# Kernel optimization log

Hardware: AMD Instinct MI355X
Metric: run time of the kernel (lower is better)

Reference implementation:

```python
import jax, jax.numpy as jnp
import numpy as np

N = 100000
E = 3200000
D_IN = 128
HEADS = 4
OUT_CH = 64


def setup_inputs() -> dict:
    key = jax.random.key(0)
    kx, ke, kw, kb = jax.random.split(key, 4)
    x = jax.random.normal(kx, (N, D_IN), dtype=jnp.float32)
    edge_index = jax.random.randint(ke, (2, E), 0, N, dtype=jnp.int64)
    # nn.Linear(in_channels, out_channels*heads): weight [out, in] in torch; store as [in, out] for x @ W
    W = jax.random.normal(kw, (D_IN, OUT_CH * HEADS), dtype=jnp.float32) * (1.0 / np.sqrt(D_IN))
    b = jax.random.normal(kb, (OUT_CH * HEADS,), dtype=jnp.float32) * 0.01
    return {"x": x, "edge_index": edge_index, "W": W, "b": b}


def reference(x, edge_index, W, b):
    src, dst = edge_index[0], edge_index[1]
    n = x.shape[0]
    # scatter-add of gathered src features into dst rows (segment sum)
    agg = jax.ops.segment_sum(x[src], dst, num_segments=n)  # [N, D_IN]
    count = jax.ops.segment_sum(jnp.ones((src.shape[0], 1), x.dtype), dst, num_segments=n)  # [N, 1]
    agg = agg / (count + 1e-8)
    # linear on (x + agg); view to [N, heads*out_channels] is a no-op reshape
    return (x + agg) @ W + b
```

## Files before the change

### kernel.cpp

```cpp
#include <hip/hip_runtime.h>

#define N_NODES 100000
#define D_IN 128
#define D_OUT 256
#define NBLK 256
#define NBKT 256
#define BSH  9
#define BNODES 512
#define NBUCKETS ((N_NODES + BNODES - 1) / BNODES)
#define CAP  19456

typedef __attribute__((ext_vector_type(8))) short short8_t;
typedef __attribute__((ext_vector_type(4))) float f32x4;

__device__ inline unsigned short f2bf_rne(float f) {
    unsigned u = __float_as_uint(f);
    u += 0x7fffu + ((u >> 16) & 1u);
    return (unsigned short)(u >> 16);
}

__global__ __launch_bounds__(256) void convert_kernel(
    const float* __restrict__ x, ushort* __restrict__ xb, int n4)
{
    int i = blockIdx.x * 256 + threadIdx.x;
    if (i < n4) {
        float4 v = ((const float4*)x)[i];
        ushort4 r;
        r.x = f2bf_rne(v.x); r.y = f2bf_rne(v.y);
        r.z = f2bf_rne(v.z); r.w = f2bf_rne(v.w);
        ((ushort4*)xb)[i] = r;
    }
}

__global__ __launch_bounds__(256) void wfrag_kernel(
    const float* __restrict__ W, short8_t* __restrict__ wfrag)
{
    int tid  = blockIdx.x * 256 + threadIdx.x;
    int lane = tid & 63;
    int fi   = tid >> 6;
    int ks   = fi >> 4, nt = fi & 15;
    int k0   = ks * 32 + (lane >> 4) * 8;
    int col  = nt * 16 + (lane & 15);
    short8_t v;
    #pragma unroll
    for (int e = 0; e < 8; e++)
        v[e] = (short)f2bf_rne(W[(size_t)(k0 + e) * D_OUT + col]);
    wfrag[tid] = v;
}

__global__ __launch_bounds__(256) void binA_hist(
    const int* __restrict__ dst, int* __restrict__ blockHist, int E, int chunk)
{
    __shared__ int h[NBKT];
    int b = blockIdx.x, t = threadIdx.x;
    h[t] = 0;
    __syncthreads();
    int e0 = b * chunk, e1 = min(e0 + chunk, E);
    for (int e = e0 + t; e < e1; e += 256)
        atomicAdd(&h[dst[e] >> BSH], 1);
    __syncthreads();
    blockHist[b * NBKT + t] = h[t];
}

__global__ __launch_bounds__(256) void binA_scan(
    int* __restrict__ blockHist, int* __restrict__ bucketTotal)
{
    __shared__ int wsum[4];
    int bucket = blockIdx.x;
    int t = threadIdx.x, lane = t & 63, w = t >> 6;
    int v = blockHist[t * NBKT + bucket];
    int s = v;
    #pragma unroll
    for (int d = 1; d < 64; d <<= 1) {
        int u = __shfl_up(s, d);
        if (lane >= d) s += u;
    }
    if (lane == 63) wsum[w] = s;
    __syncthreads();
    int wo = 0;
    for (int j = 0; j < w; j++) wo += wsum[j];
    blockHist[t * NBKT + bucket] = wo + s - v;
    if (t == 255) {
        int tot = 0;
        for (int j = 0; j < 4; j++) tot += wsum[j];
        bucketTotal[bucket] = tot;
    }
}

__global__ __launch_bounds__(256) void binA_scanbase(
    const int* __restrict__ bucketTotal, int* __restrict__ bucketBase)
{
    __shared__ int wsum[4];
    int t = threadIdx.x, lane = t & 63, w = t >> 6;
    int v = bucketTotal[t];
    int s = v;
    #pragma unroll
    for (int d = 1; d < 64; d <<= 1) {
        int u = __shfl_up(s, d);
        if (lane >= d) s += u;
    }
    if (lane == 63) wsum[w] = s;
    __syncthreads();
    int wo = 0;
    for (int j = 0; j < w; j++) wo += wsum[j];
    bucketBase[t] = wo + s - v;
}

__global__ __launch_bounds__(256) void binA_scatter(
    const int* __restrict__ src, const int* __restrict__ dst,
    const int* __restrict__ blockHist, const int* __restrict__ bucketBase,
    unsigned* __restrict__ pairs, int E, int chunk)
{
    __shared__ int offs[NBKT];
    int b = blockIdx.x, t = threadIdx.x;
    offs[t] = bucketBase[t] + blockHist[b * NBKT + t];
    __syncthreads();
    int e0 = b * chunk, e1 = min(e0 + chunk, E);
    for (int e = e0 + t; e < e1; e += 256) {
        int d = dst[e];
        int bin = d >> BSH;
        int pos = atomicAdd(&offs[bin], 1);
        pairs[pos] = ((unsigned)(d & (BNODES - 1)) << 17) | (unsigned)src[e];
    }
}

__global__ __launch_bounds__(256) void binB_sort(
    unsigned* __restrict__ pairs, const int* __restrict__ bucketBase,
    int* __restrict__ offs_g, int* __restrict__ deg_g)
{
    __shared__ unsigned stage[CAP];
    __shared__ int hist[BNODES];
    __shared__ int rank[BNODES];
    __shared__ int wsum[4];

    int b = blockIdx.x, t = threadIdx.x, lane = t & 63, w = t >> 6;
    int e0 = bucketBase[b], e1 = bucketBase[b + 1];
    int cnt = e1 - e0;
    if (cnt > CAP) cnt = CAP;

    hist[t] = 0; hist[t + 256] = 0;
    __syncthreads();

    for (int i = t; i < cnt; i += 256) {
        unsigned p = pairs[e0 + i];
        stage[i] = p;
        atomicAdd(&hist[p >> 17], 1);
    }
    __syncthreads();

    int a0 = hist[t * 2], a1 = hist[t * 2 + 1];
    int v = a0 + a1;
    int s = v;
    #pragma unroll
    for (int d = 1; d < 64; d <<= 1) {
        int u = __shfl_up(s, d);
        if (lane >= d) s += u;
    }
    if (lane == 63) wsum[w] = s;
    __syncthreads();
    int wo = 0;
    for (int j = 0; j < w; j++) wo += wsum[j];
    int excl = wo + s - v;

    rank[t * 2]     = excl;
    rank[t * 2 + 1] = excl + a0;
    int node = (b << BSH) + t * 2;
    if (node < N_NODES) {
        offs_g[node] = e0 + excl;
        deg_g[node]  = a0;
    }
    if (node + 1 < N_NODES) {
        offs_g[node + 1] = e0 + excl + a0;
        deg_g[node + 1]  = a1;
    }
    __syncthreads();

    for (int i = t; i < cnt; i += 256) {
        unsigned p = stage[i];
        int pos = atomicAdd(&rank[p >> 17], 1);
        pairs[e0 + pos] = p & 0x1FFFFu;
    }
}

template <bool USE_BF16>
__global__ __launch_bounds__(256) void fused_kernel(
    const float* __restrict__ x,
    const ushort* __restrict__ xb,
    const int* __restrict__ offs,
    const int* __restrict__ deg,
    const int* __restrict__ sorted_src,
    const short8_t* __restrict__ wfrag,
    const float* __restrict__ b,
    float* __restrict__ out)
{
    __shared__ __align__(16) ushort shb[16 * D_IN];

    int n0   = blockIdx.x * 16;
    int t    = threadIdx.x;
    int lane = t & 63;
    int w    = t >> 6;

    for (int nn = 0; nn < 4; nn++) {
        int nl = w * 4 + nn;
        int n  = n0 + nl;
        int start = offs[n];
        int d     = deg[n];
        float accx = 0.0f, accy = 0.0f;
        for (int base = 0; base < d; base += 64) {
            int m = d - base; if (m > 64) m = 64;
            int id = (lane < m) ? sorted_src[start + base + lane] : 0;
            int j = 0;
            for (; j + 4 <= m; j += 4) {
                int s0 = __builtin_amdgcn_readlane(id, j);
                int s1 = __builtin_amdgcn_readlane(id, j + 1);
                int s2 = __builtin_amdgcn_readlane(id, j + 2);
                int s3 = __builtin_amdgcn_readlane(id, j + 3);
                if (USE_BF16) {
                    ushort2 u0 = ((const ushort2*)(xb + (size_t)s0 * D_IN))[lane];
                    ushort2 u1 = ((const ushort2*)(xb + (size_t)s1 * D_IN))[lane];
                    ushort2 u2 = ((const ushort2*)(xb + (size_t)s2 * D_IN))[lane];
                    ushort2 u3 = ((const ushort2*)(xb + (size_t)s3 * D_IN))[lane];
                    accx += __uint_as_float((unsigned)u0.x << 16)
                          + __uint_as_float((unsigned)u1.x << 16)
                          + __uint_as_float((unsigned)u2.x << 16)
                          + __uint_as_float((unsigned)u3.x << 16);
                    accy += __uint_as_float((unsigned)u0.y << 16)
                          + __uint_as_float((unsigned)u1.y << 16)
                          + __uint_as_float((unsigned)u2.y << 16)
                          + __uint_as_float((unsigned)u3.y << 16);
                } else {
                    float2 v0 = ((const float2*)(x + (size_t)s0 * D_IN))[lane];
                    float2 v1 = ((const float2*)(x + (size_t)s1 * D_IN))[lane];
                    float2 v2 = ((const float2*)(x + (size_t)s2 * D_IN))[lane];
                    float2 v3 = ((const float2*)(x + (size_t)s3 * D_IN))[lane];
                    accx += v0.x + v1.x + v2.x + v3.x;
                    accy += v0.y + v1.y + v2.y + v3.y;
                }
            }
            for (; j < m; j++) {
                int s0 = __builtin_amdgcn_readlane(id, j);
                if (USE_BF16) {
                    ushort2 u0 = ((const ushort2*)(xb + (size_t)s0 * D_IN))[lane];
                    accx += __uint_as_float((unsigned)u0.x << 16);
                    accy += __uint_as_float((unsigned)u0.y << 16);
                } else {
                    float2 v0 = ((const float2*)(x + (size_t)s0 * D_IN))[lane];
                    accx += v0.x; accy += v0.y;
                }
            }
        }
        float invc = 1.0f / ((float)d + 1e-8f);
        float2 xv = ((const float2*)(x + (size_t)n * D_IN))[lane];
        float hx = xv.x + accx * invc;
        float hy = xv.y + accy * invc;
        unsigned hp = ((unsigned)f2bf_rne(hy) << 16) | (unsigned)f2bf_rne(hx);
        unsigned byteoff = ((unsigned)(nl * 256 + lane * 4)) ^ (((unsigned)nl & 7u) << 4);
        *(unsigned*)((char*)shb + byteoff) = hp;
    }
    __syncthreads();

    const int r  = lane & 15;
    const int hi = lane >> 4;

    short8_t afrag[4];
    #pragma unroll
    for (int ks = 0; ks < 4; ks++) {
        unsigned aoff = ((unsigned)(r * 256 + ks * 64 + hi * 16)) ^ (((unsigned)r & 7u) << 4);
        afrag[ks] = *(const short8_t*)((const char*)shb + aoff);
    }

    f32x4 zero = {0.0f, 0.0f, 0.0f, 0.0f};
    f32x4 acc0 = zero, acc1 = zero, acc2 = zero, acc3 = zero;
    const int nt0 = w * 4;
    #pragma unroll
    for (int ks = 0; ks < 4; ks++) {
        short8_t b0 = wfrag[(ks * 16 + nt0    ) * 64 + lane];
        short8_t b1 = wfrag[(ks * 16 + nt0 + 1) * 64 + lane];
        short8_t b2 = wfrag[(ks * 16 + nt0 + 2) * 64 + lane];
        short8_t b3 = wfrag[(ks * 16 + nt0 + 3) * 64 + lane];
        acc0 = __builtin_amdgcn_mfma_f32_16x16x32_bf16(afrag[ks], b0, acc0, 0, 0, 0);
        acc1 = __builtin_amdgcn_mfma_f32_16x16x32_bf16(afrag[ks], b1, acc1, 0, 0, 0);
        acc2 = __builtin_amdgcn_mfma_f32_16x16x32_bf16(afrag[ks], b2, acc2, 0, 0, 0);
        acc3 = __builtin_amdgcn_mfma_f32_16x16x32_bf16(afrag[ks], b3, acc3, 0, 0, 0);
    }

    #pragma unroll
    for (int nt = 0; nt < 4; nt++) {
        f32x4 a = (nt == 0) ? acc0 : (nt == 1) ? acc1 : (nt == 2) ? acc2 : acc3;
        int col = (nt0 + nt) * 16 + r;
        float bias = b[col];
        #pragma unroll
        for (int reg = 0; reg < 4; reg++) {
            int node = n0 + hi * 4 + reg;
            out[(size_t)node * D_OUT + col] = a[reg] + bias;
        }
    }
}

extern "C" void kernel_launch(void* const* d_in, const int* in_sizes, int n_in,
                              void* d_out, int out_size, void* d_ws, size_t ws_size,
                              hipStream_t stream)
{
    const float* x  = (const float*)d_in[0];
    const int*   ei = (const int*)d_in[1];
    const float* W  = (const float*)d_in[2];
    const float* b  = (const float*)d_in[3];
    float*       out = (float*)d_out;

    const int E = in_sizes[1] / 2;
    const int* src = ei;
    const int* dst = ei + E;
    const int chunk = (E + NBLK - 1) / NBLK;

    const size_t xb_bytes   = (size_t)N_NODES * D_IN * 2;
    const size_t pairs_b    = (size_t)E * 4;
    const size_t bh_b       = (size_t)NBLK * NBKT * 4;
    const size_t small_b    = (size_t)NBKT * 4;
    const size_t nodes_b    = (size_t)N_NODES * 4;
    const size_t wf_b       = (size_t)4096 * 16;
    const size_t need_bf16  = xb_bytes + pairs_b + bh_b + 2 * small_b
                            + 2 * nodes_b + wf_b;
    const bool use_bf16 = (ws_size >= need_bf16);

    char* p = (char*)d_ws;
    ushort* xb = nullptr;
    if (use_bf16) { xb = (ushort*)p; p += xb_bytes; }
    unsigned* pairs  = (unsigned*)p;  p += pairs_b;
    int* blockHist   = (int*)p;       p += bh_b;
    int* bucketTotal = (int*)p;       p += small_b;
    int* bucketBase  = (int*)p;       p += small_b;
    int* offs        = (int*)p;       p += nodes_b;
    int* deg         = (int*)p;       p += nodes_b;
    short8_t* wfrag  = (short8_t*)p;

    if (use_bf16) {
        int n4 = N_NODES * D_IN / 4;
        convert_kernel<<<dim3((n4 + 255) / 256), dim3(256), 0, stream>>>(x, xb, n4);
    }
    wfrag_kernel<<<dim3(16), dim3(256), 0, stream>>>(W, wfrag);

    binA_hist    <<<dim3(NBLK), dim3(256), 0, stream>>>(dst, blockHist, E, chunk);
    binA_scan    <<<dim3(NBKT), dim3(256), 0, stream>>>(blockHist, bucketTotal);
    binA_scanbase<<<dim3(1),    dim3(256), 0, stream>>>(bucketTotal, bucketBase);
    binA_scatter <<<dim3(NBLK), dim3(256), 0, stream>>>(
        src, dst, blockHist, bucketBase, pairs, E, chunk);
    binB_sort    <<<dim3(NBUCKETS), dim3(256), 0, stream>>>(
        pairs, bucketBase, offs, deg);

    if (use_bf16)
        fused_kernel<true><<<dim3(N_NODES / 16), dim3(256), 0, stream>>>(
            x, xb, offs, deg, (const int*)pairs, wfrag, b, out);
    else
        fused_kernel<false><<<dim3(N_NODES / 16), dim3(256), 0, stream>>>(
            x, xb, offs, deg, (const int*)pairs, wfrag, b, out);
}
```

Baseline: 405.8 us.

## Stage binning scatter through LDS to coalesce global pair writes

```diff
diff --git a/kernel.cpp b/kernel.cpp
--- a/kernel.cpp
+++ b/kernel.cpp
@@ -9,6 +9,7 @@
 #define BNODES 512
 #define NBUCKETS ((N_NODES + BNODES - 1) / BNODES)
 #define CAP  19456
+#define CAPC 12544
 
 typedef __attribute__((ext_vector_type(8))) short short8_t;
 typedef __attribute__((ext_vector_type(4))) float f32x4;
@@ -111,16 +112,64 @@
     const int* __restrict__ blockHist, const int* __restrict__ bucketBase,
     unsigned* __restrict__ pairs, int E, int chunk)
 {
-    __shared__ int offs[NBKT];
-    int b = blockIdx.x, t = threadIdx.x;
-    offs[t] = bucketBase[t] + blockHist[b * NBKT + t];
-    __syncthreads();
+    __shared__ unsigned stage[CAPC];
+    __shared__ int cnt[NBKT];
+    __shared__ int lofs[NBKT];
+    __shared__ int rankl[NBKT];
+    __shared__ int gcur[NBKT];
+    __shared__ int wsum[4];
+
+    int b = blockIdx.x, t = threadIdx.x, lane = t & 63, w = t >> 6;
     int e0 = b * chunk, e1 = min(e0 + chunk, E);
-    for (int e = e0 + t; e < e1; e += 256) {
-        int d = dst[e];
-        int bin = d >> BSH;
-        int pos = atomicAdd(&offs[bin], 1);
-        pairs[pos] = ((unsigned)(d & (BNODES - 1)) << 17) | (unsigned)src[e];
+
+    gcur[t] = bucketBase[t] + blockHist[b * NBKT + t];
+    __syncthreads();
+
+    for (int c0 = e0; c0 < e1; c0 += CAPC) {
+        int c1 = c0 + CAPC; if (c1 > e1) c1 = e1;
+
+        cnt[t] = 0;
+        __syncthreads();
+
+        for (int e = c0 + t; e < c1; e += 256)
+            atomicAdd(&cnt[dst[e] >> BSH], 1);
+        __syncthreads();
+
+        {
+            int v = cnt[t];
+            int s = v;
+            #pragma unroll
+            for (int d = 1; d < 64; d <<= 1) {
+                int u = __shfl_up(s, d);
+                if (lane >= d) s += u;
+            }
+            if (lane == 63) wsum[w] = s;
+            __syncthreads();
+            int wo = 0;
+            for (int j = 0; j < w; j++) wo += wsum[j];
+            int excl = wo + s - v;
+            lofs[t]  = excl;
+            rankl[t] = excl;
+        }
+        __syncthreads();
+
+        for (int e = c0 + t; e < c1; e += 256) {
+            int d = dst[e];
+            int bin = d >> BSH;
+            int pos = atomicAdd(&rankl[bin], 1);
+            stage[pos] = ((unsigned)(d & (BNODES - 1)) << 17) | (unsigned)src[e];
+        }
+        __syncthreads();
+
+        for (int bin = w; bin < NBKT; bin += 4) {
+            int lo = lofs[bin], c = cnt[bin], g = gcur[bin];
+            for (int i = lane; i < c; i += 64)
+                pairs[g + i] = stage[lo + i];
+        }
+        __syncthreads();
+
+        gcur[t] += cnt[t];
+        __syncthreads();
     }
 }
 
```

New measurement: 415.4 us. 1.02x slower.
